# Performance work log

Hardware: AMD Instinct MI355X
Metric: run time of the kernel (lower is better)

The kernel has to match this reference:

```python
import jax, jax.numpy as jnp
import numpy as np

IN = 4096   # input_size * 2 (is_bichar)
H = 2048    # hidden_size
C = 4096    # number of lexicon inputs


def setup_inputs() -> dict:
    key = jax.random.key(0)
    ks = jax.random.split(key, 12)
    s = 0.02
    return {
        "x": jax.random.normal(ks[0], (1, IN), jnp.float32),
        "c_input": jax.random.normal(ks[1], (C, H), jnp.float32),
        "h0": jax.random.normal(ks[2], (1, H), jnp.float32),
        "c0": jax.random.normal(ks[3], (1, H), jnp.float32),
        "W_ih": jax.random.normal(ks[4], (4 * H, IN), jnp.float32) * s,
        "b_ih": jnp.zeros((4 * H,), jnp.float32),
        "W_hh": jax.random.normal(ks[5], (4 * H, H), jnp.float32) * s,
        "b_hh": jnp.zeros((4 * H,), jnp.float32),
        "aW_ih": jax.random.normal(ks[6], (H, IN), jnp.float32) * s,
        "ab_ih": jnp.zeros((H,), jnp.float32),
        "aW_hh": jax.random.normal(ks[7], (H, H), jnp.float32) * s,
        "ab_hh": jnp.zeros((H,), jnp.float32),
    }


def reference(x, c_input, h0, c0, W_ih, b_ih, W_hh, b_hh, aW_ih, ab_ih, aW_hh, ab_hh):
    # gate pre-activations: [1, 4H]
    lstm_vec = x @ W_ih.T + b_ih + h0 @ W_hh.T + b_hh
    i, f, o, g = jnp.split(lstm_vec, 4, axis=1)
    i = jax.nn.sigmoid(i)
    f = jax.nn.sigmoid(f + 1.0)  # computed but unused when lexicon is non-empty (faithful)
    g = jnp.tanh(g)
    o = jax.nn.sigmoid(o)
    # alpha over lexicon entries: [C, H] (x-projection broadcasts over C)
    alpha = jax.nn.sigmoid(x @ aW_ih.T + ab_ih + c_input @ aW_hh.T + ab_hh)
    # exp-normalize over the (C+1) candidates per hidden unit
    w = jnp.exp(jnp.concatenate([i, alpha], axis=0))  # [C+1, H]
    w = w / w.sum(axis=0)
    merge = jnp.concatenate([g, c_input], axis=0)  # [C+1, H]
    c1 = (merge * w).sum(axis=0, keepdims=True)  # [1, H]
    h1 = o * jnp.tanh(c1)
    return h1, c1
```

## Files before the change

kernel.cpp:

```cpp
#include <hip/hip_runtime.h>
#include <hip/hip_bf16.h>
#include <cstdint>

#define HDIM 2048
#define INDIM 4096
#define CDIM 4096
#define KDIM 2048

typedef __attribute__((ext_vector_type(4))) int int4v;

__device__ __forceinline__ void gload16(const void* g, void* l) {
  __builtin_amdgcn_global_load_lds(
      (const __attribute__((address_space(1))) void*)g,
      (__attribute__((address_space(3))) void*)l, 16, 0, 0);
}

__global__ __launch_bounds__(256) void k_prep(
    const float* __restrict__ c_input, const float* __restrict__ aW_hh,
    int8_t* __restrict__ a8, int8_t* __restrict__ b8,
    float* __restrict__ dAs, float* __restrict__ dBs,
    const float* __restrict__ x, const float* __restrict__ h0,
    const float* __restrict__ W_ih, const float* __restrict__ b_ih,
    const float* __restrict__ W_hh, const float* __restrict__ b_hh,
    const float* __restrict__ aW_ih, const float* __restrict__ ab_ih,
    const float* __restrict__ ab_hh,
    float* __restrict__ i_sig, float* __restrict__ o_sig,
    float* __restrict__ g_tanh, float* __restrict__ xa2,
    float* __restrict__ accz) {
  const int t = threadIdx.x;
  const int wid = t >> 6, lane = t & 63;

  if (blockIdx.x < 1536) {
    if (blockIdx.x == 0) {
#pragma unroll
      for (int i = 0; i < 16; ++i) accz[i * 256 + t] = 0.f;
    }
    const int row = blockIdx.x * 4 + wid;
    const float* src; int8_t* dst; float* dsc; int r;
    if (row < CDIM) { src = c_input; dst = a8; dsc = dAs; r = row; }
    else            { src = aW_hh;  dst = b8; dsc = dBs; r = row - CDIM; }
    const float4* s4 = (const float4*)(src + (size_t)r * KDIM);
    float4 v[8];
#pragma unroll
    for (int it = 0; it < 8; ++it) v[it] = s4[it * 64 + lane];
    float am = 0.f;
#pragma unroll
    for (int it = 0; it < 8; ++it)
      am = fmaxf(am, fmaxf(fmaxf(fabsf(v[it].x), fabsf(v[it].y)),
                           fmaxf(fabsf(v[it].z), fabsf(v[it].w))));
#pragma unroll
    for (int off = 32; off > 0; off >>= 1) am = fmaxf(am, __shfl_xor(am, off));
    am = fmaxf(am, 1e-20f);
    const float inv = 127.0f / am;
    uint32_t* qd = (uint32_t*)(dst + (size_t)r * KDIM);
#pragma unroll
    for (int it = 0; it < 8; ++it) {
      uint32_t p = (uint32_t)(__float2int_rn(v[it].x * inv) & 0xFF)
                 | ((uint32_t)(__float2int_rn(v[it].y * inv) & 0xFF) << 8)
                 | ((uint32_t)(__float2int_rn(v[it].z * inv) & 0xFF) << 16)
                 | ((uint32_t)(__float2int_rn(v[it].w * inv) & 0xFF) << 24);
      qd[it * 64 + lane] = p;
    }
    if (lane == 0) dsc[r] = am * (1.0f / 127.0f);
    return;
  }

  const int vr = (blockIdx.x - 1536) * 4 + wid;
  const int typ = vr >> 11;
  const int h = vr & (HDIM - 1);
  float sum = 0.f;
  const float4* x4 = (const float4*)x;
  if (typ < 3) {
    const int grow = (typ == 0) ? h : (typ == 1) ? (2 * HDIM + h) : (3 * HDIM + h);
    const float4* wr4 = (const float4*)(W_ih + (size_t)grow * INDIM);
#pragma unroll
    for (int g = 0; g < 2; ++g) {
      float4 w[8];
#pragma unroll
      for (int it = 0; it < 8; ++it) w[it] = wr4[(g * 8 + it) * 64 + lane];
#pragma unroll
      for (int it = 0; it < 8; ++it) {
        float4 xv = x4[(g * 8 + it) * 64 + lane];
        sum += w[it].x * xv.x + w[it].y * xv.y + w[it].z * xv.z + w[it].w * xv.w;
      }
    }
    const float4* wh4 = (const float4*)(W_hh + (size_t)grow * HDIM);
    const float4* h4 = (const float4*)h0;
    {
      float4 w[8];
#pragma unroll
      for (int it = 0; it < 8; ++it) w[it] = wh4[it * 64 + lane];
#pragma unroll
      for (int it = 0; it < 8; ++it) {
        float4 hv = h4[it * 64 + lane];
        sum += w[it].x * hv.x + w[it].y * hv.y + w[it].z * hv.z + w[it].w * hv.w;
      }
    }
#pragma unroll
    for (int off = 32; off > 0; off >>= 1) sum += __shfl_down(sum, off);
    if (lane == 0) {
      float z = sum + b_ih[grow] + b_hh[grow];
      if (typ == 0)      i_sig[h] = 1.f / (1.f + expf(-z));
      else if (typ == 1) o_sig[h] = 1.f / (1.f + expf(-z));
      else               g_tanh[h] = tanhf(z);
    }
  } else {
    const float4* wr4 = (const float4*)(aW_ih + (size_t)h * INDIM);
#pragma unroll
    for (int g = 0; g < 2; ++g) {
      float4 w[8];
#pragma unroll
      for (int it = 0; it < 8; ++it) w[it] = wr4[(g * 8 + it) * 64 + lane];
#pragma unroll
      for (int it = 0; it < 8; ++it) {
        float4 xv = x4[(g * 8 + it) * 64 + lane];
        sum += w[it].x * xv.x + w[it].y * xv.y + w[it].z * xv.z + w[it].w * xv.w;
      }
    }
#pragma unroll
    for (int off = 32; off > 0; off >>= 1) sum += __shfl_down(sum, off);
    if (lane == 0) xa2[h] = sum + ab_ih[h] + ab_hh[h];
  }
}

__global__ __launch_bounds__(256, 2) void k_gemm_i8(
    const int8_t* __restrict__ A, const int8_t* __restrict__ B,
    const float* __restrict__ dAs, const float* __restrict__ dBs,
    const float* __restrict__ c_in, const float* __restrict__ xa2,
    float* __restrict__ acc_se, float* __restrict__ acc_sce) {
  __shared__ uint8_t As[2][16384];
  __shared__ uint8_t Bs[2][16384];
  const int t = threadIdx.x;
  const int lane = t & 63, wid = t >> 6;
  const int wr = wid >> 1, wc = wid & 1;
  const int l15 = lane & 15, l4 = lane >> 4;
  const int bm = blockIdx.x & 31, bn = blockIdx.x >> 5;
  const int m0 = bm * 128, n0 = bn * 128;

  int4v acc[4][4] = {};

  const int trow = t >> 3;
  const int tcol = ((t & 7) * 16) ^ ((trow & 7) << 4);
  const int8_t* Arow = A + (size_t)(m0 + trow) * KDIM + tcol;
  const int8_t* Brow = B + (size_t)(n0 + trow) * KDIM + tcol;

#define STAGE(buf, k0)                                                      \
  do {                                                                      \
    _Pragma("unroll")                                                       \
    for (int qq = 0; qq < 4; ++qq) {                                        \
      gload16(Arow + (size_t)qq * 32 * KDIM + (k0), As[buf] + qq * 4096 + t * 16); \
      gload16(Brow + (size_t)qq * 32 * KDIM + (k0), Bs[buf] + qq * 4096 + t * 16); \
    }                                                                       \
  } while (0)

  STAGE(0, 0);
  __syncthreads();

  int cur = 0;
  for (int ti = 0; ti < KDIM / 128; ++ti) {
    if (ti < KDIM / 128 - 1) STAGE(cur ^ 1, (ti + 1) * 128);
    int4v alo[4], ahi[4], blo[4], bhi[4];
#pragma unroll
    for (int m = 0; m < 4; ++m) {
      const int r = wr * 64 + m * 16 + l15;
      const int swz = (r & 7) << 4;
      alo[m] = *(const int4v*)(As[cur] + r * 128 + ((l4 * 16) ^ swz));
      ahi[m] = *(const int4v*)(As[cur] + r * 128 + ((64 + l4 * 16) ^ swz));
    }
#pragma unroll
    for (int n = 0; n < 4; ++n) {
      const int r = wc * 64 + n * 16 + l15;
      const int swz = (r & 7) << 4;
      blo[n] = *(const int4v*)(Bs[cur] + r * 128 + ((l4 * 16) ^ swz));
      bhi[n] = *(const int4v*)(Bs[cur] + r * 128 + ((64 + l4 * 16) ^ swz));
    }
#pragma unroll
    for (int m = 0; m < 4; ++m)
#pragma unroll
      for (int n = 0; n < 4; ++n) {
        acc[m][n] = __builtin_amdgcn_mfma_i32_16x16x64_i8(alo[m], blo[n], acc[m][n], 0, 0, 0);
        acc[m][n] = __builtin_amdgcn_mfma_i32_16x16x64_i8(ahi[m], bhi[n], acc[m][n], 0, 0, 0);
      }
    __syncthreads();
    cur ^= 1;
  }
#undef STAGE

#pragma unroll
  for (int n = 0; n < 4; ++n) {
    const int hcol = n0 + wc * 64 + n * 16 + l15;
    const float xa = xa2[hcol];
    const float db = dBs[hcol];
    float se = 0.f, sce = 0.f;
#pragma unroll
    for (int m = 0; m < 4; ++m) {
      const int jbase = m0 + wr * 64 + m * 16 + l4 * 4;
#pragma unroll
      for (int rr = 0; rr < 4; ++rr) {
        const float sc = dAs[jbase + rr] * db;
        float z = (float)acc[m][n][rr] * sc + xa;
        float s = 1.f / (1.f + __expf(-z));
        float e = __expf(s);
        se += e;
        sce += c_in[(size_t)(jbase + rr) * HDIM + hcol] * e;
      }
    }
    se += __shfl_xor(se, 16); se += __shfl_xor(se, 32);
    sce += __shfl_xor(sce, 16); sce += __shfl_xor(sce, 32);
    if (l4 == 0) {
      atomicAdd(&acc_se[hcol], se);
      atomicAdd(&acc_sce[hcol], sce);
    }
  }
}

__global__ __launch_bounds__(256) void k_final(
    const float* __restrict__ i_sig, const float* __restrict__ o_sig,
    const float* __restrict__ g_tanh, const float* __restrict__ acc_se,
    const float* __restrict__ acc_sce, float* __restrict__ out) {
  int h = blockIdx.x * 256 + threadIdx.x;
  if (h >= HDIM) return;
  float wi = expf(i_sig[h]);
  float tot = acc_se[h] + wi;
  float c1 = (acc_sce[h] + g_tanh[h] * wi) / tot;
  float h1 = o_sig[h] * tanhf(c1);
  out[h] = h1;
  out[HDIM + h] = c1;
}

extern "C" void kernel_launch(void* const* d_in, const int* in_sizes, int n_in,
                              void* d_out, int out_size, void* d_ws, size_t ws_size,
                              hipStream_t stream) {
  const float* x     = (const float*)d_in[0];
  const float* c_inp = (const float*)d_in[1];
  const float* h0    = (const float*)d_in[2];
  const float* W_ih  = (const float*)d_in[4];
  const float* b_ih  = (const float*)d_in[5];
  const float* W_hh  = (const float*)d_in[6];
  const float* b_hh  = (const float*)d_in[7];
  const float* aW_ih = (const float*)d_in[8];
  const float* ab_ih = (const float*)d_in[9];
  const float* aW_hh = (const float*)d_in[10];
  const float* ab_hh = (const float*)d_in[11];
  float* out = (float*)d_out;

  char* ws = (char*)d_ws;
  int8_t* a8 = (int8_t*)ws;
  int8_t* b8 = a8 + (size_t)CDIM * KDIM;
  float* dAs = (float*)(b8 + (size_t)HDIM * KDIM);
  float* dBs = dAs + CDIM;
  float* fb  = dBs + HDIM;
  float* i_sig   = fb;
  float* o_sig   = fb + HDIM;
  float* g_tanh  = fb + 2 * HDIM;
  float* xa2     = fb + 3 * HDIM;
  float* acc_se  = fb + 4 * HDIM;
  float* acc_sce = fb + 5 * HDIM;

  k_prep<<<1536 + 2048, 256, 0, stream>>>(
      c_inp, aW_hh, a8, b8, dAs, dBs,
      x, h0, W_ih, b_ih, W_hh, b_hh, aW_ih, ab_ih, ab_hh,
      i_sig, o_sig, g_tanh, xa2, acc_se);
  k_gemm_i8<<<(CDIM / 128) * (HDIM / 128), 256, 0, stream>>>(
      a8, b8, dAs, dBs, c_inp, xa2, acc_se, acc_sce);
  k_final<<<(HDIM + 255) / 256, 256, 0, stream>>>(i_sig, o_sig, g_tanh,
                                                  acc_se, acc_sce, out);
}
```

Before: 69.98 us.

## Move LSTM gate GEMVs into GEMM kernel and shrink GEMM K-tile

The memory-bound gate GEMVs over W_ih and W_hh move from the prep kernel into the int8 GEMM kernel as extra blocks, so their weight streaming can overlap the compute-bound MFMA tiles. The prep kernel now only quantizes and computes the alpha x-projection. The GEMM K-tile is halved to 64, which halves LDS use and raises the occupancy hint to 4 blocks per CU. The trade-off is twice as many k-iterations and barriers, and the two block types in one grid compete for CU resources.

```diff
diff --git a/kernel.cpp b/kernel.cpp
--- a/kernel.cpp
+++ b/kernel.cpp
@@ -15,18 +15,14 @@
       (__attribute__((address_space(3))) void*)l, 16, 0, 0);
 }
 
-__global__ __launch_bounds__(256) void k_prep(
+__global__ __launch_bounds__(256) void k_quant_xa2(
     const float* __restrict__ c_input, const float* __restrict__ aW_hh,
     int8_t* __restrict__ a8, int8_t* __restrict__ b8,
     float* __restrict__ dAs, float* __restrict__ dBs,
-    const float* __restrict__ x, const float* __restrict__ h0,
-    const float* __restrict__ W_ih, const float* __restrict__ b_ih,
-    const float* __restrict__ W_hh, const float* __restrict__ b_hh,
+    const float* __restrict__ x,
     const float* __restrict__ aW_ih, const float* __restrict__ ab_ih,
     const float* __restrict__ ab_hh,
-    float* __restrict__ i_sig, float* __restrict__ o_sig,
-    float* __restrict__ g_tanh, float* __restrict__ xa2,
-    float* __restrict__ accz) {
+    float* __restrict__ xa2, float* __restrict__ accz) {
   const int t = threadIdx.x;
   const int wid = t >> 6, lane = t & 63;
 
@@ -65,152 +61,156 @@
     return;
   }
 
-  const int vr = (blockIdx.x - 1536) * 4 + wid;
-  const int typ = vr >> 11;
-  const int h = vr & (HDIM - 1);
+  const int h = (blockIdx.x - 1536) * 4 + wid;
+  const float4* x4 = (const float4*)x;
+  const float4* wr4 = (const float4*)(aW_ih + (size_t)h * INDIM);
   float sum = 0.f;
-  const float4* x4 = (const float4*)x;
-  if (typ < 3) {
-    const int grow = (typ == 0) ? h : (typ == 1) ? (2 * HDIM + h) : (3 * HDIM + h);
-    const float4* wr4 = (const float4*)(W_ih + (size_t)grow * INDIM);
-#pragma unroll
-    for (int g = 0; g < 2; ++g) {
-      float4 w[8];
-#pragma unroll
-      for (int it = 0; it < 8; ++it) w[it] = wr4[(g * 8 + it) * 64 + lane];
-#pragma unroll
-      for (int it = 0; it < 8; ++it) {
-        float4 xv = x4[(g * 8 + it) * 64 + lane];
-        sum += w[it].x * xv.x + w[it].y * xv.y + w[it].z * xv.z + w[it].w * xv.w;
-      }
-    }
-    const float4* wh4 = (const float4*)(W_hh + (size_t)grow * HDIM);
-    const float4* h4 = (const float4*)h0;
-    {
-      float4 w[8];
-#pragma unroll
-      for (int it = 0; it < 8; ++it) w[it] = wh4[it * 64 + lane];
-#pragma unroll
-      for (int it = 0; it < 8; ++it) {
-        float4 hv = h4[it * 64 + lane];
-        sum += w[it].x * hv.x + w[it].y * hv.y + w[it].z * hv.z + w[it].w * hv.w;
-      }
-    }
-#pragma unroll
-    for (int off = 32; off > 0; off >>= 1) sum += __shfl_down(sum, off);
-    if (lane == 0) {
-      float z = sum + b_ih[grow] + b_hh[grow];
-      if (typ == 0)      i_sig[h] = 1.f / (1.f + expf(-z));
-      else if (typ == 1) o_sig[h] = 1.f / (1.f + expf(-z));
-      else               g_tanh[h] = tanhf(z);
-    }
-  } else {
-    const float4* wr4 = (const float4*)(aW_ih + (size_t)h * INDIM);
-#pragma unroll
-    for (int g = 0; g < 2; ++g) {
-      float4 w[8];
-#pragma unroll
-      for (int it = 0; it < 8; ++it) w[it] = wr4[(g * 8 + it) * 64 + lane];
-#pragma unroll
-      for (int it = 0; it < 8; ++it) {
-        float4 xv = x4[(g * 8 + it) * 64 + lane];
-        sum += w[it].x * xv.x + w[it].y * xv.y + w[it].z * xv.z + w[it].w * xv.w;
-      }
-    }
-#pragma unroll
-    for (int off = 32; off > 0; off >>= 1) sum += __shfl_down(sum, off);
-    if (lane == 0) xa2[h] = sum + ab_ih[h] + ab_hh[h];
-  }
-}
-
-__global__ __launch_bounds__(256, 2) void k_gemm_i8(
+#pragma unroll
+  for (int g = 0; g < 2; ++g) {
+    float4 w[8];
+#pragma unroll
+    for (int it = 0; it < 8; ++it) w[it] = wr4[(g * 8 + it) * 64 + lane];
+#pragma unroll
+    for (int it = 0; it < 8; ++it) {
+      float4 xv = x4[(g * 8 + it) * 64 + lane];
+      sum += w[it].x * xv.x + w[it].y * xv.y + w[it].z * xv.z + w[it].w * xv.w;
+    }
+  }
+#pragma unroll
+  for (int off = 32; off > 0; off >>= 1) sum += __shfl_down(sum, off);
+  if (lane == 0) xa2[h] = sum + ab_ih[h] + ab_hh[h];
+}
+
+__global__ __launch_bounds__(256, 4) void k_gemm_gemv(
     const int8_t* __restrict__ A, const int8_t* __restrict__ B,
     const float* __restrict__ dAs, const float* __restrict__ dBs,
     const float* __restrict__ c_in, const float* __restrict__ xa2,
-    float* __restrict__ acc_se, float* __restrict__ acc_sce) {
-  __shared__ uint8_t As[2][16384];
-  __shared__ uint8_t Bs[2][16384];
+    float* __restrict__ acc_se, float* __restrict__ acc_sce,
+    const float* __restrict__ x, const float* __restrict__ h0,
+    const float* __restrict__ W_ih, const float* __restrict__ b_ih,
+    const float* __restrict__ W_hh, const float* __restrict__ b_hh,
+    float* __restrict__ i_sig, float* __restrict__ o_sig,
+    float* __restrict__ g_tanh) {
+  __shared__ uint8_t As[2][8192];
+  __shared__ uint8_t Bs[2][8192];
   const int t = threadIdx.x;
   const int lane = t & 63, wid = t >> 6;
-  const int wr = wid >> 1, wc = wid & 1;
-  const int l15 = lane & 15, l4 = lane >> 4;
-  const int bm = blockIdx.x & 31, bn = blockIdx.x >> 5;
-  const int m0 = bm * 128, n0 = bn * 128;
-
-  int4v acc[4][4] = {};
-
-  const int trow = t >> 3;
-  const int tcol = ((t & 7) * 16) ^ ((trow & 7) << 4);
-  const int8_t* Arow = A + (size_t)(m0 + trow) * KDIM + tcol;
-  const int8_t* Brow = B + (size_t)(n0 + trow) * KDIM + tcol;
-
-#define STAGE(buf, k0)                                                      \
-  do {                                                                      \
-    _Pragma("unroll")                                                       \
-    for (int qq = 0; qq < 4; ++qq) {                                        \
-      gload16(Arow + (size_t)qq * 32 * KDIM + (k0), As[buf] + qq * 4096 + t * 16); \
-      gload16(Brow + (size_t)qq * 32 * KDIM + (k0), Bs[buf] + qq * 4096 + t * 16); \
-    }                                                                       \
-  } while (0)
-
-  STAGE(0, 0);
-  __syncthreads();
-
-  int cur = 0;
-  for (int ti = 0; ti < KDIM / 128; ++ti) {
-    if (ti < KDIM / 128 - 1) STAGE(cur ^ 1, (ti + 1) * 128);
-    int4v alo[4], ahi[4], blo[4], bhi[4];
-#pragma unroll
-    for (int m = 0; m < 4; ++m) {
-      const int r = wr * 64 + m * 16 + l15;
-      const int swz = (r & 7) << 4;
-      alo[m] = *(const int4v*)(As[cur] + r * 128 + ((l4 * 16) ^ swz));
-      ahi[m] = *(const int4v*)(As[cur] + r * 128 + ((64 + l4 * 16) ^ swz));
-    }
+
+  if (blockIdx.x < 512) {
+    const int wr = wid >> 1, wc = wid & 1;
+    const int l15 = lane & 15, l4 = lane >> 4;
+    const int bm = blockIdx.x & 31, bn = blockIdx.x >> 5;
+    const int m0 = bm * 128, n0 = bn * 128;
+
+    int4v acc[4][4] = {};
+
+    const int trow = t >> 2;
+    const int tcol = ((t & 3) * 16) ^ ((trow & 3) << 4);
+    const int8_t* Arow = A + (size_t)(m0 + trow) * KDIM + tcol;
+    const int8_t* Brow = B + (size_t)(n0 + trow) * KDIM + tcol;
+
+#define STAGE(buf, k0)                                                          \
+    do {                                                                        \
+      _Pragma("unroll")                                                         \
+      for (int qq = 0; qq < 2; ++qq) {                                          \
+        gload16(Arow + (size_t)qq * 64 * KDIM + (k0), As[buf] + qq * 4096 + t * 16); \
+        gload16(Brow + (size_t)qq * 64 * KDIM + (k0), Bs[buf] + qq * 4096 + t * 16); \
+      }                                                                         \
+    } while (0)
+
+    STAGE(0, 0);
+    __syncthreads();
+
+    int cur = 0;
+    for (int ti = 0; ti < KDIM / 64; ++ti) {
+      if (ti < KDIM / 64 - 1) STAGE(cur ^ 1, (ti + 1) * 64);
+      int4v af[4], bfr[4];
+#pragma unroll
+      for (int m = 0; m < 4; ++m) {
+        const int r = wr * 64 + m * 16 + l15;
+        af[m] = *(const int4v*)(As[cur] + r * 64 + ((l4 * 16) ^ ((r & 3) << 4)));
+      }
+#pragma unroll
+      for (int n = 0; n < 4; ++n) {
+        const int r = wc * 64 + n * 16 + l15;
+        bfr[n] = *(const int4v*)(Bs[cur] + r * 64 + ((l4 * 16) ^ ((r & 3) << 4)));
+      }
+#pragma unroll
+      for (int m = 0; m < 4; ++m)
+#pragma unroll
+        for (int n = 0; n < 4; ++n)
+          acc[m][n] = __builtin_amdgcn_mfma_i32_16x16x64_i8(af[m], bfr[n], acc[m][n], 0, 0, 0);
+      __syncthreads();
+      cur ^= 1;
+    }
+#undef STAGE
+
 #pragma unroll
     for (int n = 0; n < 4; ++n) {
-      const int r = wc * 64 + n * 16 + l15;
-      const int swz = (r & 7) << 4;
-      blo[n] = *(const int4v*)(Bs[cur] + r * 128 + ((l4 * 16) ^ swz));
-      bhi[n] = *(const int4v*)(Bs[cur] + r * 128 + ((64 + l4 * 16) ^ swz));
-    }
-#pragma unroll
-    for (int m = 0; m < 4; ++m)
-#pragma unroll
-      for (int n = 0; n < 4; ++n) {
-        acc[m][n] = __builtin_amdgcn_mfma_i32_16x16x64_i8(alo[m], blo[n], acc[m][n], 0, 0, 0);
-        acc[m][n] = __builtin_amdgcn_mfma_i32_16x16x64_i8(ahi[m], bhi[n], acc[m][n], 0, 0, 0);
-      }
-    __syncthreads();
-    cur ^= 1;
-  }
-#undef STAGE
-
-#pragma unroll
-  for (int n = 0; n < 4; ++n) {
-    const int hcol = n0 + wc * 64 + n * 16 + l15;
-    const float xa = xa2[hcol];
-    const float db = dBs[hcol];
-    float se = 0.f, sce = 0.f;
-#pragma unroll
-    for (int m = 0; m < 4; ++m) {
-      const int jbase = m0 + wr * 64 + m * 16 + l4 * 4;
-#pragma unroll
-      for (int rr = 0; rr < 4; ++rr) {
-        const float sc = dAs[jbase + rr] * db;
-        float z = (float)acc[m][n][rr] * sc + xa;
-        float s = 1.f / (1.f + __expf(-z));
-        float e = __expf(s);
-        se += e;
-        sce += c_in[(size_t)(jbase + rr) * HDIM + hcol] * e;
-      }
-    }
-    se += __shfl_xor(se, 16); se += __shfl_xor(se, 32);
-    sce += __shfl_xor(sce, 16); sce += __shfl_xor(sce, 32);
-    if (l4 == 0) {
-      atomicAdd(&acc_se[hcol], se);
-      atomicAdd(&acc_sce[hcol], sce);
-    }
+      const int hcol = n0 + wc * 64 + n * 16 + l15;
+      const float xa = xa2[hcol];
+      const float db = dBs[hcol];
+      float se = 0.f, sce = 0.f;
+#pragma unroll
+      for (int m = 0; m < 4; ++m) {
+        const int jbase = m0 + wr * 64 + m * 16 + l4 * 4;
+#pragma unroll
+        for (int rr = 0; rr < 4; ++rr) {
+          const float sc = dAs[jbase + rr] * db;
+          float z = (float)acc[m][n][rr] * sc + xa;
+          float s = 1.f / (1.f + __expf(-z));
+          float e = __expf(s);
+          se += e;
+          sce += c_in[(size_t)(jbase + rr) * HDIM + hcol] * e;
+        }
+      }
+      se += __shfl_xor(se, 16); se += __shfl_xor(se, 32);
+      sce += __shfl_xor(sce, 16); sce += __shfl_xor(sce, 32);
+      if (l4 == 0) {
+        atomicAdd(&acc_se[hcol], se);
+        atomicAdd(&acc_sce[hcol], sce);
+      }
+    }
+    return;
+  }
+
+  const int vr = (blockIdx.x - 512) * 4 + wid;
+  const int typ = vr >> 11;
+  const int h = vr & (HDIM - 1);
+  const int grow = (typ == 0) ? h : (typ == 1) ? (2 * HDIM + h) : (3 * HDIM + h);
+  float sum = 0.f;
+  const float4* x4 = (const float4*)x;
+  const float4* wr4 = (const float4*)(W_ih + (size_t)grow * INDIM);
+#pragma unroll
+  for (int g = 0; g < 2; ++g) {
+    float4 w[8];
+#pragma unroll
+    for (int it = 0; it < 8; ++it) w[it] = wr4[(g * 8 + it) * 64 + lane];
+#pragma unroll
+    for (int it = 0; it < 8; ++it) {
+      float4 xv = x4[(g * 8 + it) * 64 + lane];
+      sum += w[it].x * xv.x + w[it].y * xv.y + w[it].z * xv.z + w[it].w * xv.w;
+    }
+  }
+  {
+    const float4* wh4 = (const float4*)(W_hh + (size_t)grow * HDIM);
+    const float4* h4 = (const float4*)h0;
+    float4 w[8];
+#pragma unroll
+    for (int it = 0; it < 8; ++it) w[it] = wh4[it * 64 + lane];
+#pragma unroll
+    for (int it = 0; it < 8; ++it) {
+      float4 hv = h4[it * 64 + lane];
+      sum += w[it].x * hv.x + w[it].y * hv.y + w[it].z * hv.z + w[it].w * hv.w;
+    }
+  }
+#pragma unroll
+  for (int off = 32; off > 0; off >>= 1) sum += __shfl_down(sum, off);
+  if (lane == 0) {
+    float z = sum + b_ih[grow] + b_hh[grow];
+    if (typ == 0)      i_sig[h] = 1.f / (1.f + expf(-z));
+    else if (typ == 1) o_sig[h] = 1.f / (1.f + expf(-z));
+    else               g_tanh[h] = tanhf(z);
   }
 }
 
@@ -257,12 +257,11 @@
   float* acc_se  = fb + 4 * HDIM;
   float* acc_sce = fb + 5 * HDIM;
 
-  k_prep<<<1536 + 2048, 256, 0, stream>>>(
-      c_inp, aW_hh, a8, b8, dAs, dBs,
-      x, h0, W_ih, b_ih, W_hh, b_hh, aW_ih, ab_ih, ab_hh,
-      i_sig, o_sig, g_tanh, xa2, acc_se);
-  k_gemm_i8<<<(CDIM / 128) * (HDIM / 128), 256, 0, stream>>>(
-      a8, b8, dAs, dBs, c_inp, xa2, acc_se, acc_sce);
+  k_quant_xa2<<<2048, 256, 0, stream>>>(
+      c_inp, aW_hh, a8, b8, dAs, dBs, x, aW_ih, ab_ih, ab_hh, xa2, acc_se);
+  k_gemm_gemv<<<512 + 1536, 256, 0, stream>>>(
+      a8, b8, dAs, dBs, c_inp, xa2, acc_se, acc_sce,
+      x, h0, W_ih, b_ih, W_hh, b_hh, i_sig, o_sig, g_tanh);
   k_final<<<(HDIM + 255) / 256, 256, 0, stream>>>(i_sig, o_sig, g_tanh,
                                                   acc_se, acc_sce, out);
 }
```

Result: faster. 65.64 us (-6.2%).
